# Kernel optimization log

Measured on AMD Instinct MI355X. Metric: run time of the kernel, lower is better.

## Reference

```python
import jax, jax.numpy as jnp
import numpy as np

N_NODES = 100000
N_EDGES = 600000
HIDDEN = 128


def setup_inputs() -> dict:
    key = jax.random.key(0)
    ks = jax.random.split(key, 5)
    x = jax.random.normal(ks[0], (N_NODES, HIDDEN), dtype=jnp.float32)
    edge_index = jax.random.randint(ks[1], (2, N_EDGES), 0, N_NODES, dtype=jnp.int64)
    edge_weight = jax.random.uniform(ks[2], (N_EDGES,), dtype=jnp.float32)
    # MLP params: Linear(2*H+1 -> H), ReLU, Linear(H -> 1)
    W1 = jax.random.normal(ks[3], (2 * HIDDEN + 1, HIDDEN), dtype=jnp.float32) * (1.0 / np.sqrt(2 * HIDDEN + 1))
    b1 = jnp.zeros((HIDDEN,), dtype=jnp.float32)
    W2 = jax.random.normal(ks[4], (HIDDEN, 1), dtype=jnp.float32) * (1.0 / np.sqrt(HIDDEN))
    b2 = jnp.zeros((1,), dtype=jnp.float32)
    return {"x": x, "edge_index": edge_index, "edge_weight": edge_weight,
            "W1": W1, "b1": b1, "W2": W2, "b2": b2}


def reference(x, edge_index, edge_weight, W1, b1, W2, b2):
    num_nodes = x.shape[0]
    src = edge_index[0]
    tgt = edge_index[1]
    h_src = x[src]                      # [E, H] gather
    h_tgt = x[tgt]                      # [E, H] gather
    w = edge_weight[:, None]            # [E, 1]
    concat = jnp.concatenate([h_src, h_tgt, w], axis=-1)   # [E, 2H+1]
    hidden = jax.nn.relu(concat @ W1 + b1)                 # [E, H]
    scores = (hidden @ W2 + b2)[:, 0]                      # [E]
    # NOTE: the original _softmax_edge's max-pass uses index_put_(accumulate=True)
    # on a -inf buffer, so every touched entry stays -inf and is then replaced by 0;
    # the net effect is NO max subtraction. Faithful math: plain exp / segment_sum.
    exp_scores = jnp.exp(scores)
    sum_exp = jax.ops.segment_sum(exp_scores, tgt, num_segments=num_nodes)
    sum_exp = jnp.maximum(sum_exp, 1e-12)
    alpha = exp_scores / sum_exp[tgt]                      # [E]
    out = jax.ops.segment_sum(alpha[:, None] * h_src, tgt, num_segments=num_nodes)
    return x + out
```

## Files before the change

kernel.cpp:

```cpp
#include <hip/hip_runtime.h>
#include <hip/hip_bf16.h>

#define N_NODES 100000
#define N_EDGES 600000
#define HID 128
#define SCAN_NB ((N_NODES + 255) / 256)


typedef short bf16x8 __attribute__((ext_vector_type(8)));
typedef float f32x4  __attribute__((ext_vector_type(4)));

__device__ inline unsigned short f2bf(float v) {
    __hip_bfloat16 h = __float2bfloat16(v);
    return *(unsigned short*)&h;
}
__device__ inline float bf2f(unsigned short s) {
    unsigned int u = (unsigned int)s << 16;
    return __uint_as_float(u);
}
__device__ inline float2 bfpair(unsigned int u) {
    float lo = __uint_as_float(u << 16);
    float hi = __uint_as_float(u & 0xffff0000u);
    return make_float2(lo, hi);
}

__global__ __launch_bounds__(256) void k_prepB(const float* __restrict__ W1,
                                               unsigned short* __restrict__ Bh,
                                               unsigned short* __restrict__ Bl)
{
    int idx = blockIdx.x * 256 + threadIdx.x;
    int n = idx & 255;
    int k = idx >> 8;
    float v = (n < HID) ? W1[k * HID + n] : W1[(HID + k) * HID + (n - HID)];
    unsigned short h = f2bf(v);
    float r = v - bf2f(h);
    unsigned short l = f2bf(r);
    int dst = (k >> 5) * 8192 + n * 32 + (k & 31);
    Bh[dst] = h;
    Bl[dst] = l;
}

__global__ __launch_bounds__(256) void k_gemm(const float* __restrict__ x,
                                              const unsigned short* __restrict__ BhG,
                                              const unsigned short* __restrict__ BlG,
                                              unsigned short* __restrict__ zbuf,
                                              unsigned short* __restrict__ y2buf)
{
    __shared__ unsigned short Ah[64 * 32];
    __shared__ unsigned short Al[64 * 32];

    const int tid  = threadIdx.x;
    const int bm   = blockIdx.x * 64;
    const int wave = tid >> 6;
    const int lane = tid & 63;
    const int q    = lane >> 4;
    const int ln   = lane & 15;

    f32x4 acc[4][4] = {};

    for (int ks = 0; ks < 4; ++ks) {
        const int k0 = ks * 32;
        #pragma unroll
        for (int it = 0; it < 2; ++it) {
            int t   = tid + it * 256;
            int row = t >> 3;
            int f4  = t & 7;
            int gm  = bm + row;
            float4 v = make_float4(0.f, 0.f, 0.f, 0.f);
            if (gm < N_NODES) v = *(const float4*)&x[(size_t)gm * HID + k0 + f4 * 4];
            unsigned short h0 = f2bf(v.x), h1 = f2bf(v.y), h2 = f2bf(v.z), h3 = f2bf(v.w);
            unsigned int ph0 = (unsigned int)h0 | ((unsigned int)h1 << 16);
            unsigned int ph1 = (unsigned int)h2 | ((unsigned int)h3 << 16);
            unsigned short l0 = f2bf(v.x - bf2f(h0)), l1 = f2bf(v.y - bf2f(h1));
            unsigned short l2 = f2bf(v.z - bf2f(h2)), l3 = f2bf(v.w - bf2f(h3));
            unsigned int pl0 = (unsigned int)l0 | ((unsigned int)l1 << 16);
            unsigned int pl1 = (unsigned int)l2 | ((unsigned int)l3 << 16);
            int o = row * 32 + f4 * 4;
            *(uint2*)&Ah[o] = make_uint2(ph0, ph1);
            *(uint2*)&Al[o] = make_uint2(pl0, pl1);
            if (gm < N_NODES) {
                *(uint2*)&zbuf[(size_t)gm * 256 + 128 + k0 + f4 * 4] = make_uint2(ph0, ph1);
            }
        }
        __syncthreads();

        bf16x8 ah[4], al[4], bh[4], bl[4];
        #pragma unroll
        for (int mt = 0; mt < 4; ++mt) {
            int o = (mt * 16 + ln) * 32 + q * 8;
            ah[mt] = *(const bf16x8*)&Ah[o];
            al[mt] = *(const bf16x8*)&Al[o];
        }
        #pragma unroll
        for (int nt = 0; nt < 4; ++nt) {
            int o = ks * 8192 + (wave * 64 + nt * 16 + ln) * 32 + q * 8;
            bh[nt] = *(const bf16x8*)&BhG[o];
            bl[nt] = *(const bf16x8*)&BlG[o];
        }
        #pragma unroll
        for (int mt = 0; mt < 4; ++mt) {
            #pragma unroll
            for (int nt = 0; nt < 4; ++nt) {
                acc[mt][nt] = __builtin_amdgcn_mfma_f32_16x16x32_bf16(ah[mt], bh[nt], acc[mt][nt], 0, 0, 0);
                acc[mt][nt] = __builtin_amdgcn_mfma_f32_16x16x32_bf16(ah[mt], bl[nt], acc[mt][nt], 0, 0, 0);
                acc[mt][nt] = __builtin_amdgcn_mfma_f32_16x16x32_bf16(al[mt], bh[nt], acc[mt][nt], 0, 0, 0);
            }
        }
        __syncthreads();
    }

    #pragma unroll
    for (int mt = 0; mt < 4; ++mt) {
        #pragma unroll
        for (int r = 0; r < 4; ++r) {
            int row = bm + mt * 16 + q * 4 + r;
            if (row < N_NODES) {
                #pragma unroll
                for (int nt = 0; nt < 4; ++nt) {
                    int col = wave * 64 + nt * 16 + ln;
                    unsigned short v = f2bf(acc[mt][nt][r]);
                    if (col < 128) zbuf[(size_t)row * 256 + col] = v;
                    else           y2buf[(size_t)row * 128 + (col - 128)] = v;
                }
            }
        }
    }
}

__global__ __launch_bounds__(256) void k_count(const int* __restrict__ ei,
                                               int* __restrict__ deg)
{
    int e = blockIdx.x * blockDim.x + threadIdx.x;
    if (e < N_EDGES) atomicAdd(&deg[ei[N_EDGES + e]], 1);
}

__global__ __launch_bounds__(256) void k_partial(const int* __restrict__ deg,
                                                 int* __restrict__ partial)
{
    __shared__ int s[256];
    int t = threadIdx.x;
    int idx = blockIdx.x * 256 + t;
    s[t] = (idx < N_NODES) ? deg[idx] : 0;
    __syncthreads();
    #pragma unroll
    for (int off = 128; off > 0; off >>= 1) {
        if (t < off) s[t] += s[t + off];
        __syncthreads();
    }
    if (t == 0) partial[blockIdx.x] = s[0];
}

__global__ __launch_bounds__(512) void k_scanp(const int* __restrict__ partial,
                                               int* __restrict__ pbase)
{
    __shared__ int s[512];
    int t = threadIdx.x;
    int v = (t < SCAN_NB) ? partial[t] : 0;
    s[t] = v;
    __syncthreads();
    #pragma unroll
    for (int off = 1; off < 512; off <<= 1) {
        int u = (t >= off) ? s[t - off] : 0;
        __syncthreads();
        s[t] += u;
        __syncthreads();
    }
    if (t < SCAN_NB) pbase[t] = s[t] - v;
}

__global__ __launch_bounds__(256) void k_rowptr(const int* __restrict__ deg,
                                                const int* __restrict__ pbase,
                                                int* __restrict__ rowptr,
                                                int* __restrict__ cursor)
{
    __shared__ int s[256];
    int t = threadIdx.x;
    int b = blockIdx.x;
    int idx = b * 256 + t;
    int v = (idx < N_NODES) ? deg[idx] : 0;
    s[t] = v;
    __syncthreads();
    #pragma unroll
    for (int off = 1; off < 256; off <<= 1) {
        int u = (t >= off) ? s[t - off] : 0;
        __syncthreads();
        s[t] += u;
        __syncthreads();
    }
    if (idx < N_NODES) {
        int r = pbase[b] + s[t] - v;
        rowptr[idx] = r;
        cursor[idx] = r;
    }
    if (idx == 0) rowptr[N_NODES] = N_EDGES;
}

__global__ __launch_bounds__(256) void k_fill(const int* __restrict__ ei,
                                              const float* __restrict__ ew,
                                              int* __restrict__ cursor,
                                              int* __restrict__ esrc,
                                              float* __restrict__ ewb)
{
    int e = blockIdx.x * blockDim.x + threadIdx.x;
    if (e >= N_EDGES) return;
    int tgt = ei[N_EDGES + e];
    int pos = atomicAdd(&cursor[tgt], 1);
    esrc[pos] = ei[e];
    ewb[pos] = ew[e];
}

__global__ __launch_bounds__(256) void k_fused(const unsigned int* __restrict__ zu,
                                               const unsigned int* __restrict__ y2u,
                                               const int* __restrict__ rowptr,
                                               const int* __restrict__ esrc,
                                               const float* __restrict__ ewb,
                                               const float* __restrict__ x,
                                               const float* __restrict__ W1,
                                               const float* __restrict__ b1,
                                               const float* __restrict__ W2,
                                               const float* __restrict__ b2,
                                               float* __restrict__ out)
{
    int n = (blockIdx.x * blockDim.x + threadIdx.x) >> 6;
    int lane = threadIdx.x & 63;
    if (n >= N_NODES) return;
    int c0 = lane * 2;

    float2 y2 = bfpair(y2u[(size_t)n * 64 + lane]);
    float2 bv = *(const float2*)&b1[c0];
    float2 pre = make_float2(y2.x + bv.x, y2.y + bv.y);
    float2 wr = *(const float2*)&W1[256 * HID + c0];
    float2 w2 = *(const float2*)&W2[c0];
    float b2v = b2[0];

    int beg = rowptr[n], end = rowptr[n + 1];
    float accx = 0.f, accy = 0.f, denom = 0.f;

    int i = beg;
    for (; i + 2 <= end; i += 2) {
        int src0 = esrc[i],     src1 = esrc[i + 1];
        float w0 = ewb[i],      w1 = ewb[i + 1];
        unsigned int ua0 = zu[(size_t)src0 * 128 + lane];
        unsigned int ux0 = zu[(size_t)src0 * 128 + 64 + lane];
        unsigned int ua1 = zu[(size_t)src1 * 128 + lane];
        unsigned int ux1 = zu[(size_t)src1 * 128 + 64 + lane];
        float2 a0 = bfpair(ua0), a1 = bfpair(ua1);
        float h00 = fmaxf(a0.x + pre.x + w0 * wr.x, 0.f);
        float h01 = fmaxf(a0.y + pre.y + w0 * wr.y, 0.f);
        float h10 = fmaxf(a1.x + pre.x + w1 * wr.x, 0.f);
        float h11 = fmaxf(a1.y + pre.y + w1 * wr.y, 0.f);
        float p0 = h00 * w2.x + h01 * w2.y;
        float p1 = h10 * w2.x + h11 * w2.y;
        #pragma unroll
        for (int m = 32; m > 0; m >>= 1) {
            p0 += __shfl_xor(p0, m, 64);
            p1 += __shfl_xor(p1, m, 64);
        }
        float es0 = __expf(p0 + b2v);
        float es1 = __expf(p1 + b2v);
        float2 xf0 = bfpair(ux0), xf1 = bfpair(ux1);
        accx = fmaf(es0, xf0.x, accx); accy = fmaf(es0, xf0.y, accy);
        accx = fmaf(es1, xf1.x, accx); accy = fmaf(es1, xf1.y, accy);
        denom += es0 + es1;
    }
    if (i < end) {
        int src0 = esrc[i];
        float w0 = ewb[i];
        unsigned int ua0 = zu[(size_t)src0 * 128 + lane];
        unsigned int ux0 = zu[(size_t)src0 * 128 + 64 + lane];
        float2 a0 = bfpair(ua0);
        float h00 = fmaxf(a0.x + pre.x + w0 * wr.x, 0.f);
        float h01 = fmaxf(a0.y + pre.y + w0 * wr.y, 0.f);
        float p0 = h00 * w2.x + h01 * w2.y;
        #pragma unroll
        for (int m = 32; m > 0; m >>= 1) p0 += __shfl_xor(p0, m, 64);
        float es0 = __expf(p0 + b2v);
        float2 xf0 = bfpair(ux0);
        accx = fmaf(es0, xf0.x, accx); accy = fmaf(es0, xf0.y, accy);
        denom += es0;
    }

    float2 xt = *(const float2*)&x[(size_t)n * HID + c0];
    float inv = 1.0f / fmaxf(denom, 1e-12f);
    out[(size_t)n * HID + c0]     = xt.x + accx * inv;
    out[(size_t)n * HID + c0 + 1] = xt.y + accy * inv;
}

extern "C" void kernel_launch(void* const* d_in, const int* in_sizes, int n_in,
                              void* d_out, int out_size, void* d_ws, size_t ws_size,
                              hipStream_t stream) {
    const float* x  = (const float*)d_in[0];
    const int*   ei = (const int*)d_in[1];
    const float* ew = (const float*)d_in[2];
    const float* W1 = (const float*)d_in[3];
    const float* b1 = (const float*)d_in[4];
    const float* W2 = (const float*)d_in[5];
    const float* b2 = (const float*)d_in[6];
    float* out = (float*)d_out;
    char* ws = (char*)d_ws;

    const size_t deg_b    = 400000;
    const size_t rowptr_b = 400016;
    const size_t cursor_b = 400000;
    const size_t esrc_b   = 2400000;
    const size_t ewb_b    = 2400000;
    const size_t part_b   = 1568;
    const size_t pb_b     = 1568;
    const size_t Bh_b     = 65536;
    const size_t Bl_b     = 65536;

    char* p = ws;
    int* deg      = (int*)p;             p += deg_b;
    int* rowptr   = (int*)p;             p += rowptr_b;
    int* cursor   = (int*)p;             p += cursor_b;
    int* esrc     = (int*)p;             p += esrc_b;
    float* ewb    = (float*)p;           p += ewb_b;
    int* partial  = (int*)p;             p += part_b;
    int* pbase    = (int*)p;             p += pb_b;
    unsigned short* BhG = (unsigned short*)p;  p += Bh_b;
    unsigned short* BlG = (unsigned short*)p;  p += Bl_b;
    unsigned short* zbuf  = (unsigned short*)p;  p += (size_t)N_NODES * 256 * 2;
    unsigned short* y2buf = (unsigned short*)p;

    const int edge_blocks = (N_EDGES + 255) / 256;
    const int node_wave_blocks = (N_NODES * 64 + 255) / 256;
    const int gemm_blocks = (N_NODES + 63) / 64;

    hipMemsetAsync(deg, 0, deg_b, stream);
    hipLaunchKernelGGL(k_prepB, dim3(128), dim3(256), 0, stream, W1, BhG, BlG);
    hipLaunchKernelGGL(k_count, dim3(edge_blocks), dim3(256), 0, stream, ei, deg);
    hipLaunchKernelGGL(k_partial, dim3(SCAN_NB), dim3(256), 0, stream, deg, partial);
    hipLaunchKernelGGL(k_scanp, dim3(1), dim3(512), 0, stream, partial, pbase);
    hipLaunchKernelGGL(k_rowptr, dim3(SCAN_NB), dim3(256), 0, stream, deg, pbase, rowptr, cursor);
    hipLaunchKernelGGL(k_fill, dim3(edge_blocks), dim3(256), 0, stream,
                       ei, ew, cursor, esrc, ewb);
    hipLaunchKernelGGL(k_gemm, dim3(gemm_blocks), dim3(256), 0, stream, x, BhG, BlG, zbuf, y2buf);
    hipLaunchKernelGGL(k_fused, dim3(node_wave_blocks), dim3(256), 0, stream,
                       (const unsigned int*)zbuf, (const unsigned int*)y2buf,
                       rowptr, esrc, ewb, x, W1, b1, W2, b2, out);
}
```

Baseline: 301.0 us.

## Pack edge data, split wave across edges, prefetch GEMM loads, fold memset

Four separate changes. The memset of the degree array is folded into the weight-prep kernel, saving one launch. The GEMM now prefetches the next K-slice of x into registers before the MFMA work so the global load latency overlaps compute. Edge source and weight are packed into one uint2 array so each edge is one 8-byte load. The fused node kernel splits each wave into two 32-lane halves that each handle different edges with 4 channels per lane, which shortens the shuffle reductions and issues wider loads, at the cost of a cross-half reduction and some masked padding iterations.

```diff
diff --git a/kernel.cpp b/kernel.cpp
--- a/kernel.cpp
+++ b/kernel.cpp
@@ -24,20 +24,24 @@
     return make_float2(lo, hi);
 }
 
-__global__ __launch_bounds__(256) void k_prepB(const float* __restrict__ W1,
-                                               unsigned short* __restrict__ Bh,
-                                               unsigned short* __restrict__ Bl)
+__global__ __launch_bounds__(256) void k_prep(const float* __restrict__ W1,
+                                              unsigned short* __restrict__ Bh,
+                                              unsigned short* __restrict__ Bl,
+                                              int* __restrict__ deg)
 {
     int idx = blockIdx.x * 256 + threadIdx.x;
-    int n = idx & 255;
-    int k = idx >> 8;
-    float v = (n < HID) ? W1[k * HID + n] : W1[(HID + k) * HID + (n - HID)];
-    unsigned short h = f2bf(v);
-    float r = v - bf2f(h);
-    unsigned short l = f2bf(r);
-    int dst = (k >> 5) * 8192 + n * 32 + (k & 31);
-    Bh[dst] = h;
-    Bl[dst] = l;
+    if (idx < N_NODES) deg[idx] = 0;
+    if (idx < 32768) {
+        int n = idx & 255;
+        int k = idx >> 8;
+        float v = (n < HID) ? W1[k * HID + n] : W1[(HID + k) * HID + (n - HID)];
+        unsigned short h = f2bf(v);
+        float r = v - bf2f(h);
+        unsigned short l = f2bf(r);
+        int dst = (k >> 5) * 8192 + n * 32 + (k & 31);
+        Bh[dst] = h;
+        Bl[dst] = l;
+    }
 }
 
 __global__ __launch_bounds__(256) void k_gemm(const float* __restrict__ x,
@@ -56,18 +60,27 @@
     const int q    = lane >> 4;
     const int ln   = lane & 15;
 
+    const int rowA = tid >> 3;
+    const int rowB = rowA + 32;
+    const int f4   = tid & 7;
+    const int gmA  = bm + rowA;
+    const int gmB  = bm + rowB;
+    const bool okA = gmA < N_NODES;
+    const bool okB = gmB < N_NODES;
+    const float* pxA = &x[(size_t)gmA * HID + f4 * 4];
+    const float* pxB = &x[(size_t)gmB * HID + f4 * 4];
+
     f32x4 acc[4][4] = {};
+
+    float4 vA = make_float4(0.f,0.f,0.f,0.f), vB = vA;
+    float4 vAn = vA, vBn = vA;
+    if (okA) vA = *(const float4*)pxA;
+    if (okB) vB = *(const float4*)pxB;
 
     for (int ks = 0; ks < 4; ++ks) {
         const int k0 = ks * 32;
-        #pragma unroll
-        for (int it = 0; it < 2; ++it) {
-            int t   = tid + it * 256;
-            int row = t >> 3;
-            int f4  = t & 7;
-            int gm  = bm + row;
-            float4 v = make_float4(0.f, 0.f, 0.f, 0.f);
-            if (gm < N_NODES) v = *(const float4*)&x[(size_t)gm * HID + k0 + f4 * 4];
+        {
+            float4 v = vA;
             unsigned short h0 = f2bf(v.x), h1 = f2bf(v.y), h2 = f2bf(v.z), h3 = f2bf(v.w);
             unsigned int ph0 = (unsigned int)h0 | ((unsigned int)h1 << 16);
             unsigned int ph1 = (unsigned int)h2 | ((unsigned int)h3 << 16);
@@ -75,14 +88,31 @@
             unsigned short l2 = f2bf(v.z - bf2f(h2)), l3 = f2bf(v.w - bf2f(h3));
             unsigned int pl0 = (unsigned int)l0 | ((unsigned int)l1 << 16);
             unsigned int pl1 = (unsigned int)l2 | ((unsigned int)l3 << 16);
-            int o = row * 32 + f4 * 4;
+            int o = rowA * 32 + f4 * 4;
             *(uint2*)&Ah[o] = make_uint2(ph0, ph1);
             *(uint2*)&Al[o] = make_uint2(pl0, pl1);
-            if (gm < N_NODES) {
-                *(uint2*)&zbuf[(size_t)gm * 256 + 128 + k0 + f4 * 4] = make_uint2(ph0, ph1);
-            }
-        }
-        __syncthreads();
+            if (okA) *(uint2*)&zbuf[(size_t)gmA * 256 + 128 + k0 + f4 * 4] = make_uint2(ph0, ph1);
+        }
+        {
+            float4 v = vB;
+            unsigned short h0 = f2bf(v.x), h1 = f2bf(v.y), h2 = f2bf(v.z), h3 = f2bf(v.w);
+            unsigned int ph0 = (unsigned int)h0 | ((unsigned int)h1 << 16);
+            unsigned int ph1 = (unsigned int)h2 | ((unsigned int)h3 << 16);
+            unsigned short l0 = f2bf(v.x - bf2f(h0)), l1 = f2bf(v.y - bf2f(h1));
+            unsigned short l2 = f2bf(v.z - bf2f(h2)), l3 = f2bf(v.w - bf2f(h3));
+            unsigned int pl0 = (unsigned int)l0 | ((unsigned int)l1 << 16);
+            unsigned int pl1 = (unsigned int)l2 | ((unsigned int)l3 << 16);
+            int o = rowB * 32 + f4 * 4;
+            *(uint2*)&Ah[o] = make_uint2(ph0, ph1);
+            *(uint2*)&Al[o] = make_uint2(pl0, pl1);
+            if (okB) *(uint2*)&zbuf[(size_t)gmB * 256 + 128 + k0 + f4 * 4] = make_uint2(ph0, ph1);
+        }
+        __syncthreads();
+
+        if (ks < 3) {
+            vAn = okA ? *(const float4*)(pxA + (ks + 1) * 32) : make_float4(0.f,0.f,0.f,0.f);
+            vBn = okB ? *(const float4*)(pxB + (ks + 1) * 32) : make_float4(0.f,0.f,0.f,0.f);
+        }
 
         bf16x8 ah[4], al[4], bh[4], bl[4];
         #pragma unroll
@@ -107,6 +137,7 @@
             }
         }
         __syncthreads();
+        vA = vAn; vB = vBn;
     }
 
     #pragma unroll
@@ -198,22 +229,19 @@
 __global__ __launch_bounds__(256) void k_fill(const int* __restrict__ ei,
                                               const float* __restrict__ ew,
                                               int* __restrict__ cursor,
-                                              int* __restrict__ esrc,
-                                              float* __restrict__ ewb)
+                                              uint2* __restrict__ eprs)
 {
     int e = blockIdx.x * blockDim.x + threadIdx.x;
     if (e >= N_EDGES) return;
     int tgt = ei[N_EDGES + e];
     int pos = atomicAdd(&cursor[tgt], 1);
-    esrc[pos] = ei[e];
-    ewb[pos] = ew[e];
+    eprs[pos] = make_uint2((unsigned int)ei[e], __float_as_uint(ew[e]));
 }
 
 __global__ __launch_bounds__(256) void k_fused(const unsigned int* __restrict__ zu,
                                                const unsigned int* __restrict__ y2u,
                                                const int* __restrict__ rowptr,
-                                               const int* __restrict__ esrc,
-                                               const float* __restrict__ ewb,
+                                               const uint2* __restrict__ eprs,
                                                const float* __restrict__ x,
                                                const float* __restrict__ W1,
                                                const float* __restrict__ b1,
@@ -224,66 +252,87 @@
     int n = (blockIdx.x * blockDim.x + threadIdx.x) >> 6;
     int lane = threadIdx.x & 63;
     if (n >= N_NODES) return;
-    int c0 = lane * 2;
-
-    float2 y2 = bfpair(y2u[(size_t)n * 64 + lane]);
-    float2 bv = *(const float2*)&b1[c0];
-    float2 pre = make_float2(y2.x + bv.x, y2.y + bv.y);
-    float2 wr = *(const float2*)&W1[256 * HID + c0];
-    float2 w2 = *(const float2*)&W2[c0];
+    int sl = lane & 31;
+    int hl = lane >> 5;
+    int c0 = sl * 4;
+
+    uint2 uy2 = *(const uint2*)&y2u[(size_t)n * 64 + sl * 2];
+    float2 y2a = bfpair(uy2.x), y2b = bfpair(uy2.y);
+    float4 bv = *(const float4*)&b1[c0];
+    float4 wr = *(const float4*)&W1[256 * HID + c0];
+    float4 w2 = *(const float4*)&W2[c0];
+    float pc0 = y2a.x + bv.x, pc1 = y2a.y + bv.y;
+    float pc2 = y2b.x + bv.z, pc3 = y2b.y + bv.w;
     float b2v = b2[0];
 
     int beg = rowptr[n], end = rowptr[n + 1];
-    float accx = 0.f, accy = 0.f, denom = 0.f;
-
-    int i = beg;
-    for (; i + 2 <= end; i += 2) {
-        int src0 = esrc[i],     src1 = esrc[i + 1];
-        float w0 = ewb[i],      w1 = ewb[i + 1];
-        unsigned int ua0 = zu[(size_t)src0 * 128 + lane];
-        unsigned int ux0 = zu[(size_t)src0 * 128 + 64 + lane];
-        unsigned int ua1 = zu[(size_t)src1 * 128 + lane];
-        unsigned int ux1 = zu[(size_t)src1 * 128 + 64 + lane];
-        float2 a0 = bfpair(ua0), a1 = bfpair(ua1);
-        float h00 = fmaxf(a0.x + pre.x + w0 * wr.x, 0.f);
-        float h01 = fmaxf(a0.y + pre.y + w0 * wr.y, 0.f);
-        float h10 = fmaxf(a1.x + pre.x + w1 * wr.x, 0.f);
-        float h11 = fmaxf(a1.y + pre.y + w1 * wr.y, 0.f);
-        float p0 = h00 * w2.x + h01 * w2.y;
-        float p1 = h10 * w2.x + h11 * w2.y;
-        #pragma unroll
-        for (int m = 32; m > 0; m >>= 1) {
-            p0 += __shfl_xor(p0, m, 64);
-            p1 += __shfl_xor(p1, m, 64);
-        }
-        float es0 = __expf(p0 + b2v);
-        float es1 = __expf(p1 + b2v);
-        float2 xf0 = bfpair(ux0), xf1 = bfpair(ux1);
-        accx = fmaf(es0, xf0.x, accx); accy = fmaf(es0, xf0.y, accy);
-        accx = fmaf(es1, xf1.x, accx); accy = fmaf(es1, xf1.y, accy);
-        denom += es0 + es1;
-    }
-    if (i < end) {
-        int src0 = esrc[i];
-        float w0 = ewb[i];
-        unsigned int ua0 = zu[(size_t)src0 * 128 + lane];
-        unsigned int ux0 = zu[(size_t)src0 * 128 + 64 + lane];
-        float2 a0 = bfpair(ua0);
-        float h00 = fmaxf(a0.x + pre.x + w0 * wr.x, 0.f);
-        float h01 = fmaxf(a0.y + pre.y + w0 * wr.y, 0.f);
-        float p0 = h00 * w2.x + h01 * w2.y;
-        #pragma unroll
-        for (int m = 32; m > 0; m >>= 1) p0 += __shfl_xor(p0, m, 64);
-        float es0 = __expf(p0 + b2v);
-        float2 xf0 = bfpair(ux0);
-        accx = fmaf(es0, xf0.x, accx); accy = fmaf(es0, xf0.y, accy);
-        denom += es0;
-    }
-
-    float2 xt = *(const float2*)&x[(size_t)n * HID + c0];
-    float inv = 1.0f / fmaxf(denom, 1e-12f);
-    out[(size_t)n * HID + c0]     = xt.x + accx * inv;
-    out[(size_t)n * HID + c0 + 1] = xt.y + accy * inv;
+    float acc0 = 0.f, acc1 = 0.f, acc2 = 0.f, acc3 = 0.f, denom = 0.f;
+
+    for (int i = beg; i < end; i += 4) {
+        int idxA = i + hl;
+        int idxB = i + 2 + hl;
+        bool vA = idxA < end;
+        bool vB = idxB < end;
+        int iA = vA ? idxA : (end - 1);
+        int iB = vB ? idxB : (end - 1);
+        uint2 epA = eprs[iA];
+        uint2 epB = eprs[iB];
+        size_t bA = (size_t)epA.x * 128;
+        size_t bB = (size_t)epB.x * 128;
+        float wA = __uint_as_float(epA.y);
+        float wB = __uint_as_float(epB.y);
+        uint2 uyA = *(const uint2*)&zu[bA + sl * 2];
+        uint2 uxA = *(const uint2*)&zu[bA + 64 + sl * 2];
+        uint2 uyB = *(const uint2*)&zu[bB + sl * 2];
+        uint2 uxB = *(const uint2*)&zu[bB + 64 + sl * 2];
+
+        float2 aA0 = bfpair(uyA.x), aA1 = bfpair(uyA.y);
+        float hA0 = fmaxf(fmaf(wA, wr.x, aA0.x + pc0), 0.f);
+        float hA1 = fmaxf(fmaf(wA, wr.y, aA0.y + pc1), 0.f);
+        float hA2 = fmaxf(fmaf(wA, wr.z, aA1.x + pc2), 0.f);
+        float hA3 = fmaxf(fmaf(wA, wr.w, aA1.y + pc3), 0.f);
+        float pA = hA0 * w2.x + hA1 * w2.y + hA2 * w2.z + hA3 * w2.w;
+
+        float2 aB0 = bfpair(uyB.x), aB1 = bfpair(uyB.y);
+        float hB0 = fmaxf(fmaf(wB, wr.x, aB0.x + pc0), 0.f);
+        float hB1 = fmaxf(fmaf(wB, wr.y, aB0.y + pc1), 0.f);
+        float hB2 = fmaxf(fmaf(wB, wr.z, aB1.x + pc2), 0.f);
+        float hB3 = fmaxf(fmaf(wB, wr.w, aB1.y + pc3), 0.f);
+        float pB = hB0 * w2.x + hB1 * w2.y + hB2 * w2.z + hB3 * w2.w;
+
+        #pragma unroll
+        for (int m = 1; m <= 16; m <<= 1) {
+            pA += __shfl_xor(pA, m, 64);
+            pB += __shfl_xor(pB, m, 64);
+        }
+        float esA = __expf(pA + b2v); if (!vA) esA = 0.f;
+        float esB = __expf(pB + b2v); if (!vB) esB = 0.f;
+
+        float2 xA0 = bfpair(uxA.x), xA1 = bfpair(uxA.y);
+        float2 xB0 = bfpair(uxB.x), xB1 = bfpair(uxB.y);
+        acc0 = fmaf(esA, xA0.x, acc0); acc0 = fmaf(esB, xB0.x, acc0);
+        acc1 = fmaf(esA, xA0.y, acc1); acc1 = fmaf(esB, xB0.y, acc1);
+        acc2 = fmaf(esA, xA1.x, acc2); acc2 = fmaf(esB, xB1.x, acc2);
+        acc3 = fmaf(esA, xA1.y, acc3); acc3 = fmaf(esB, xB1.y, acc3);
+        denom += esA + esB;
+    }
+
+    acc0 += __shfl_xor(acc0, 32, 64);
+    acc1 += __shfl_xor(acc1, 32, 64);
+    acc2 += __shfl_xor(acc2, 32, 64);
+    acc3 += __shfl_xor(acc3, 32, 64);
+    denom += __shfl_xor(denom, 32, 64);
+
+    if (hl == 0) {
+        float4 xt = *(const float4*)&x[(size_t)n * HID + c0];
+        float inv = 1.0f / fmaxf(denom, 1e-12f);
+        float4 o;
+        o.x = xt.x + acc0 * inv;
+        o.y = xt.y + acc1 * inv;
+        o.z = xt.z + acc2 * inv;
+        o.w = xt.w + acc3 * inv;
+        *(float4*)&out[(size_t)n * HID + c0] = o;
+    }
 }
 
 extern "C" void kernel_launch(void* const* d_in, const int* in_sizes, int n_in,
@@ -302,8 +351,7 @@
     const size_t deg_b    = 400000;
     const size_t rowptr_b = 400016;
     const size_t cursor_b = 400000;
-    const size_t esrc_b   = 2400000;
-    const size_t ewb_b    = 2400000;
+    const size_t eprs_b   = 4800000;
     const size_t part_b   = 1568;
     const size_t pb_b     = 1568;
     const size_t Bh_b     = 65536;
@@ -313,8 +361,7 @@
     int* deg      = (int*)p;             p += deg_b;
     int* rowptr   = (int*)p;             p += rowptr_b;
     int* cursor   = (int*)p;             p += cursor_b;
-    int* esrc     = (int*)p;             p += esrc_b;
-    float* ewb    = (float*)p;           p += ewb_b;
+    uint2* eprs   = (uint2*)p;           p += eprs_b;
     int* partial  = (int*)p;             p += part_b;
     int* pbase    = (int*)p;             p += pb_b;
     unsigned short* BhG = (unsigned short*)p;  p += Bh_b;
@@ -326,16 +373,14 @@
     const int node_wave_blocks = (N_NODES * 64 + 255) / 256;
     const int gemm_blocks = (N_NODES + 63) / 64;
 
-    hipMemsetAsync(deg, 0, deg_b, stream);
-    hipLaunchKernelGGL(k_prepB, dim3(128), dim3(256), 0, stream, W1, BhG, BlG);
+    hipLaunchKernelGGL(k_prep, dim3(SCAN_NB), dim3(256), 0, stream, W1, BhG, BlG, deg);
     hipLaunchKernelGGL(k_count, dim3(edge_blocks), dim3(256), 0, stream, ei, deg);
     hipLaunchKernelGGL(k_partial, dim3(SCAN_NB), dim3(256), 0, stream, deg, partial);
     hipLaunchKernelGGL(k_scanp, dim3(1), dim3(512), 0, stream, partial, pbase);
     hipLaunchKernelGGL(k_rowptr, dim3(SCAN_NB), dim3(256), 0, stream, deg, pbase, rowptr, cursor);
-    hipLaunchKernelGGL(k_fill, dim3(edge_blocks), dim3(256), 0, stream,
-                       ei, ew, cursor, esrc, ewb);
+    hipLaunchKernelGGL(k_fill, dim3(edge_blocks), dim3(256), 0, stream, ei, ew, cursor, eprs);
     hipLaunchKernelGGL(k_gemm, dim3(gemm_blocks), dim3(256), 0, stream, x, BhG, BlG, zbuf, y2buf);
     hipLaunchKernelGGL(k_fused, dim3(node_wave_blocks), dim3(256), 0, stream,
                        (const unsigned int*)zbuf, (const unsigned int*)y2buf,
-                       rowptr, esrc, ewb, x, W1, b1, W2, b2, out);
-}
+                       rowptr, eprs, x, W1, b1, W2, b2, out);
+}
```

After: 288.4 us. 1.04x faster.
